# Performance work log

Hardware: AMD Instinct MI355X
Metric: run time of the kernel (lower is better)

## Reference

```python
import jax, jax.numpy as jnp
import numpy as np


def _warp_nn(img, flow):
    """Nearest-neighbor warp of one sample.
    img:  [C, D, H, W] channels to deform
    flow: [3, D, H, W] voxel displacements for dims (D, H, W)
    out(p) = img(round(p + flow(p))), indices clamped to the volume.
    """
    D, H, W = img.shape[1:]
    gd = jnp.arange(D, dtype=flow.dtype)[:, None, None]
    gh = jnp.arange(H, dtype=flow.dtype)[None, :, None]
    gw = jnp.arange(W, dtype=flow.dtype)[None, None, :]
    id_ = jnp.clip(jnp.round(gd + flow[0]), 0, D - 1).astype(jnp.int32)
    ih = jnp.clip(jnp.round(gh + flow[1]), 0, H - 1).astype(jnp.int32)
    iw = jnp.clip(jnp.round(gw + flow[2]), 0, W - 1).astype(jnp.int32)
    return img[:, id_, ih, iw]  # gather, [C, D, H, W]


def reference(x, num_steps):
    # scaling: v = x / 2**num_steps
    B, C = x.shape[0], x.shape[1]
    spatial = x.shape[2:]
    v = x / (2.0 ** num_steps)
    # squaring: v <- v + warp(v, v), applied per 3-channel flow group
    warp = jax.vmap(jax.vmap(_warp_nn))  # over batch, then over groups
    for _ in range(num_steps):
        groups = v.reshape(B, C // 3, 3, *spatial)
        vdef = warp(groups, groups).reshape(v.shape)
        v = v + vdef
    return v


def setup_inputs() -> dict:
    key = jax.random.key(0)
    # displacement field in voxel units; scaled so post-scaling steps still move voxels
    x = jax.random.normal(key, (2, 3, 128, 160, 160), dtype=jnp.float32) * 8.0
    return {"x": x, "num_steps": 6}
```

## Files before the change

### kernel.cpp

```cpp
#include <hip/hip_runtime.h>

#define BB 2
#define DD 128
#define HH 160
#define WW 160
constexpr int S   = DD * HH * WW;
constexpr int PL  = HH * WW;
constexpr int K   = 4;
constexpr int VPB = 256 * K;
constexpr int TPP = PL / VPB;
constexpr int NT  = BB * DD * TPP;
constexpr int PER_XCD = NT / 8;

struct __attribute__((packed, aligned(4))) f3 { float x, y, z; };

__device__ __forceinline__ void clamp_idx(int d, int h, int w,
                                          float f0, float f1, float f2,
                                          int& od, int& oh, int& ow, int& lin) {
    od = (int)fminf(fmaxf(rintf((float)d + f0), 0.0f), (float)(DD - 1));
    oh = (int)fminf(fmaxf(rintf((float)h + f1), 0.0f), (float)(HH - 1));
    ow = (int)fminf(fmaxf(rintf((float)w + f2), 0.0f), (float)(WW - 1));
    lin = (od * HH + oh) * WW + ow;
}

template <bool SOA>
__device__ __forceinline__ void load3(const float* __restrict__ v, int b, int idx,
                                      float scale, float* o) {
    if constexpr (SOA) {
        int s = b * 3 * S + idx;
        o[0] = v[s] * scale; o[1] = v[s + S] * scale; o[2] = v[s + 2 * S] * scale;
    } else {
        f3 t = *(const f3*)(v + (b * S + idx) * 3);
        o[0] = t.x; o[1] = t.y; o[2] = t.z;
    }
}

template <bool IN_SOA, bool OUT_SOA>
__global__ __launch_bounds__(256) void fused2_k(const float* __restrict__ vin,
                                                float* __restrict__ vout,
                                                float scale) {
    int t  = blockIdx.x;
    int nb = (t >> 3) + (t & 7) * PER_XCD;
    int b  = nb / (DD * TPP);
    int r  = nb - b * (DD * TPP);
    int d  = r / TPP;
    int ip0 = (r - d * TPP) * VPB + threadIdx.x;

    int   p[K], h[K], w[K];
    float a[K][3];
#pragma unroll
    for (int k = 0; k < K; ++k) {
        int ip = ip0 + k * 256;
        w[k] = ip % WW; h[k] = ip / WW;
        p[k] = d * PL + ip;
        load3<IN_SOA>(vin, b, p[k], scale, a[k]);
    }
    int r0i[K];
#pragma unroll
    for (int k = 0; k < K; ++k) {
        int rd, rh, rw;
        clamp_idx(d, h[k], w[k], a[k][0], a[k][1], a[k][2], rd, rh, rw, r0i[k]);
    }
    float g[K][3];
#pragma unroll
    for (int k = 0; k < K; ++k) load3<IN_SOA>(vin, b, r0i[k], scale, g[k]);
    float v1[K][3];
    int r1d[K], r1h[K], r1w[K], r1i[K];
#pragma unroll
    for (int k = 0; k < K; ++k) {
        v1[k][0] = a[k][0] + g[k][0];
        v1[k][1] = a[k][1] + g[k][1];
        v1[k][2] = a[k][2] + g[k][2];
        clamp_idx(d, h[k], w[k], v1[k][0], v1[k][1], v1[k][2],
                  r1d[k], r1h[k], r1w[k], r1i[k]);
    }
    float bb[K][3];
#pragma unroll
    for (int k = 0; k < K; ++k) load3<IN_SOA>(vin, b, r1i[k], scale, bb[k]);
    int r2i[K];
#pragma unroll
    for (int k = 0; k < K; ++k) {
        int rd, rh, rw;
        clamp_idx(r1d[k], r1h[k], r1w[k], bb[k][0], bb[k][1], bb[k][2],
                  rd, rh, rw, r2i[k]);
    }
    float h2[K][3];
#pragma unroll
    for (int k = 0; k < K; ++k) load3<IN_SOA>(vin, b, r2i[k], scale, h2[k]);
#pragma unroll
    for (int k = 0; k < K; ++k) {
        float o0 = v1[k][0] + (bb[k][0] + h2[k][0]);
        float o1 = v1[k][1] + (bb[k][1] + h2[k][1]);
        float o2 = v1[k][2] + (bb[k][2] + h2[k][2]);
        if constexpr (OUT_SOA) {
            int s = b * 3 * S + p[k];
            vout[s] = o0; vout[s + S] = o1; vout[s + 2 * S] = o2;
        } else {
            f3 v{o0, o1, o2};
            *(f3*)(vout + (b * S + p[k]) * 3) = v;
        }
    }
}

extern "C" void kernel_launch(void* const* d_in, const int* in_sizes, int n_in,
                              void* d_out, int out_size, void* d_ws, size_t ws_size,
                              hipStream_t stream) {
    const float* x = (const float*)d_in[0];
    float* out = (float*)d_out;
    float* ws  = (float*)d_ws;

    fused2_k<true,  false><<<NT, 256, 0, stream>>>(x,   out, 1.0f / 64.0f);
    fused2_k<false, false><<<NT, 256, 0, stream>>>(out, ws,  1.0f);
    fused2_k<false, true ><<<NT, 256, 0, stream>>>(ws,  out, 1.0f);
}
```

Measured before the change: 273.8 us.

## Fuse four squaring steps into one recursive gather kernel with self-hit skip

Replaces the three two-step kernels with a recursive template that evaluates N squaring steps per voxel by walking the gather tree. The first launch fuses four steps directly from the SoA input and the second fuses the remaining two, which cuts one full pass over the volume. When the gathered index equals the query index, the load is replaced by reuse of the already held value. The cost is that the number of gathers per voxel grows exponentially with N (about fifteen dependent random loads for N=4) and register pressure rises, in exchange for fewer global round trips.

```diff
diff --git a/kernel.cpp b/kernel.cpp
--- a/kernel.cpp
+++ b/kernel.cpp
@@ -35,8 +35,37 @@
     }
 }
 
-template <bool IN_SOA, bool OUT_SOA>
-__global__ __launch_bounds__(256) void fused2_k(const float* __restrict__ vin,
+template <int N, int MASKN, bool SOA>
+__device__ __forceinline__ void eval(const float* __restrict__ vin, int b, float scale,
+                                     int qd, int qh, int qw, int qi,
+                                     const float* v0q, float* out) {
+    if constexpr (N == 0) {
+        out[0] = v0q[0]; out[1] = v0q[1]; out[2] = v0q[2];
+    } else {
+        float a[3];
+        eval<N - 1, MASKN, SOA>(vin, b, scale, qd, qh, qw, qi, v0q, a);
+        int rd, rh, rw, ri;
+        clamp_idx(qd, qh, qw, a[0], a[1], a[2], rd, rh, rw, ri);
+        float v0r[3];
+        if constexpr (N <= MASKN) {
+            if (ri != qi) {
+                load3<SOA>(vin, b, ri, scale, v0r);
+            } else {
+                v0r[0] = v0q[0]; v0r[1] = v0q[1]; v0r[2] = v0q[2];
+            }
+        } else {
+            load3<SOA>(vin, b, ri, scale, v0r);
+        }
+        float g[3];
+        eval<N - 1, MASKN, SOA>(vin, b, scale, rd, rh, rw, ri, v0r, g);
+        out[0] = a[0] + g[0];
+        out[1] = a[1] + g[1];
+        out[2] = a[2] + g[2];
+    }
+}
+
+template <int NSTEP, int MASKN, bool IN_SOA, bool OUT_SOA>
+__global__ __launch_bounds__(256) void squash_k(const float* __restrict__ vin,
                                                 float* __restrict__ vout,
                                                 float scale) {
     int t  = blockIdx.x;
@@ -47,56 +76,25 @@
     int ip0 = (r - d * TPP) * VPB + threadIdx.x;
 
     int   p[K], h[K], w[K];
-    float a[K][3];
+    float a0[K][3];
 #pragma unroll
     for (int k = 0; k < K; ++k) {
         int ip = ip0 + k * 256;
         w[k] = ip % WW; h[k] = ip / WW;
         p[k] = d * PL + ip;
-        load3<IN_SOA>(vin, b, p[k], scale, a[k]);
+        load3<IN_SOA>(vin, b, p[k], scale, a0[k]);
     }
-    int r0i[K];
+    float o[K][3];
+#pragma unroll
+    for (int k = 0; k < K; ++k)
+        eval<NSTEP, MASKN, IN_SOA>(vin, b, scale, d, h[k], w[k], p[k], a0[k], o[k]);
 #pragma unroll
     for (int k = 0; k < K; ++k) {
-        int rd, rh, rw;
-        clamp_idx(d, h[k], w[k], a[k][0], a[k][1], a[k][2], rd, rh, rw, r0i[k]);
-    }
-    float g[K][3];
-#pragma unroll
-    for (int k = 0; k < K; ++k) load3<IN_SOA>(vin, b, r0i[k], scale, g[k]);
-    float v1[K][3];
-    int r1d[K], r1h[K], r1w[K], r1i[K];
-#pragma unroll
-    for (int k = 0; k < K; ++k) {
-        v1[k][0] = a[k][0] + g[k][0];
-        v1[k][1] = a[k][1] + g[k][1];
-        v1[k][2] = a[k][2] + g[k][2];
-        clamp_idx(d, h[k], w[k], v1[k][0], v1[k][1], v1[k][2],
-                  r1d[k], r1h[k], r1w[k], r1i[k]);
-    }
-    float bb[K][3];
-#pragma unroll
-    for (int k = 0; k < K; ++k) load3<IN_SOA>(vin, b, r1i[k], scale, bb[k]);
-    int r2i[K];
-#pragma unroll
-    for (int k = 0; k < K; ++k) {
-        int rd, rh, rw;
-        clamp_idx(r1d[k], r1h[k], r1w[k], bb[k][0], bb[k][1], bb[k][2],
-                  rd, rh, rw, r2i[k]);
-    }
-    float h2[K][3];
-#pragma unroll
-    for (int k = 0; k < K; ++k) load3<IN_SOA>(vin, b, r2i[k], scale, h2[k]);
-#pragma unroll
-    for (int k = 0; k < K; ++k) {
-        float o0 = v1[k][0] + (bb[k][0] + h2[k][0]);
-        float o1 = v1[k][1] + (bb[k][1] + h2[k][1]);
-        float o2 = v1[k][2] + (bb[k][2] + h2[k][2]);
         if constexpr (OUT_SOA) {
             int s = b * 3 * S + p[k];
-            vout[s] = o0; vout[s + S] = o1; vout[s + 2 * S] = o2;
+            vout[s] = o[k][0]; vout[s + S] = o[k][1]; vout[s + 2 * S] = o[k][2];
         } else {
-            f3 v{o0, o1, o2};
+            f3 v{o[k][0], o[k][1], o[k][2]};
             *(f3*)(vout + (b * S + p[k]) * 3) = v;
         }
     }
@@ -109,7 +107,6 @@
     float* out = (float*)d_out;
     float* ws  = (float*)d_ws;
 
-    fused2_k<true,  false><<<NT, 256, 0, stream>>>(x,   out, 1.0f / 64.0f);
-    fused2_k<false, false><<<NT, 256, 0, stream>>>(out, ws,  1.0f);
-    fused2_k<false, true ><<<NT, 256, 0, stream>>>(ws,  out, 1.0f);
+    squash_k<4, 3, true,  false><<<NT, 256, 0, stream>>>(x,  ws,  1.0f / 64.0f);
+    squash_k<2, 0, false, true ><<<NT, 256, 0, stream>>>(ws, out, 1.0f);
 }
```

New measurement: 301.3 us. 10.0% more time.
